# Kernel optimization log

Measured on AMD Instinct MI355X. Metric: run time of the kernel, lower is better.

## Reference

```python
import jax, jax.numpy as jnp
import numpy as np

N = 51200      # num nodes
E = 614400     # num edges
G = 256        # num graphs
T = 8          # num target capsules (GCNConv heads)
D = 128        # in_channels == out_channels
ROUTES = 3     # num_routes
BN_EPS = 1e-5


def squash(s):
    # s: (..., D). v = |s|^2/(1+|s|^2) * s/|s|
    s2 = jnp.sum(s * s, axis=-1, keepdims=True)
    return (s2 / (1.0 + s2)) * s * jax.lax.rsqrt(s2 + 1e-16)


def setup_inputs() -> dict:
    key = jax.random.key(0)
    k0, k1, k2, k3 = jax.random.split(key, 4)
    x = jax.random.normal(k0, (N, D), dtype=jnp.float32)
    edge_index = jax.random.randint(k1, (2, E), 0, N, dtype=jnp.int32)
    batch = jnp.sort(jax.random.randint(k2, (N,), 0, G, dtype=jnp.int32))
    edge_weight = jnp.ones((E,), dtype=jnp.float32)
    gamma = jnp.ones((D,), dtype=jnp.float32)
    beta = jnp.zeros((D,), dtype=jnp.float32)
    W = jax.random.normal(k3, (T, D, D), dtype=jnp.float32) * (1.0 / np.sqrt(D))
    bias = jnp.zeros((T, D), dtype=jnp.float32)
    return {"x": x, "edge_weight": edge_weight, "gamma": gamma, "beta": beta,
            "W": W, "bias": bias, "edge_index": edge_index, "batch": batch}


def reference(x, edge_weight, gamma, beta, W, bias, edge_index, batch):
    n = x.shape[0]
    row, col = edge_index[0], edge_index[1]

    # BatchNorm1d (training-mode batch stats)
    mu = jnp.mean(x, axis=0)
    var = jnp.var(x, axis=0)
    x = (x - mu) * jax.lax.rsqrt(var + BN_EPS) * gamma + beta

    # --- GCNConv per target capsule (PyG gcn_norm with self-loops) ---
    sl = jnp.arange(n, dtype=row.dtype)
    row_sl = jnp.concatenate([row, sl])
    col_sl = jnp.concatenate([col, sl])
    w_sl = jnp.concatenate([edge_weight, jnp.ones((n,), x.dtype)])
    deg = jax.ops.segment_sum(w_sl, col_sl, num_segments=n)
    dis = jnp.where(deg > 0, jax.lax.rsqrt(jnp.maximum(deg, 1e-12)), 0.0)
    norm = dis[row_sl] * w_sl * dis[col_sl]          # (E+N,)

    xW = jnp.einsum('nd,tdo->nto', x, W)             # (N, T, D)
    caps = []
    for t in range(T):  # small fixed loop over capsule heads keeps edge msgs at (E+N, D)
        msg = norm[:, None] * xW[row_sl, t]          # (E+N, D)
        caps.append(jax.ops.segment_sum(msg, col_sl, num_segments=n) + bias[t])
    u_hat = jnp.stack(caps, axis=1)                  # (N, T, D)

    # --- dynamic routing ---
    node_deg = jax.ops.segment_sum(edge_weight, row, num_segments=n)  # original edges, no self loops
    b = jnp.broadcast_to(node_deg[:, None, None], (n, T, 1))
    u_det = jax.lax.stop_gradient(u_hat)
    for _ in range(ROUTES - 1):
        c = jax.nn.softmax(b, axis=1)                               # (N, T, 1)
        s = jax.ops.segment_sum(c * u_det, batch, num_segments=G)   # (G, T, D)
        v = squash(s)[batch]                                        # (N, T, D)
        b = b + jnp.sum(u_det * v, axis=-1, keepdims=True)

    c = jax.nn.softmax(b, axis=1)
    s = jax.ops.segment_sum(c * u_hat, batch, num_segments=G)        # (G, T, D)
    cnt = jax.ops.segment_sum(jnp.ones((n,), x.dtype), batch, num_segments=G)
    x_mean = jax.ops.segment_sum(x, batch, num_segments=G) / jnp.maximum(cnt, 1.0)[:, None]
    s = s + x_mean[:, None, :]
    v = squash(s)
    # final_layer=True: per-capsule L2 norm -> (G, T)
    return jnp.sqrt(jnp.sum(v * v, axis=-1) + 1e-16)
```

## Files before the change

### kernel.cpp

```cpp
#include <hip/hip_runtime.h>
#include <hip/hip_bf16.h>
#include <math.h>

#define N_NODES 51200
#define N_EDGES 614400
#define N_GRAPHS 256
#define T_CAPS 8
#define D_DIM 128
#define BN_EPS 1e-5f
#define RCAP 352
#define NBUCK 200
#define BCAP 4096
#define EPB 1024
#define SBLK 600

__device__ inline float waveReduceSum(float v) {
#pragma unroll
  for (int off = 1; off < 64; off <<= 1) v += __shfl_xor(v, off, 64);
  return v;
}
__device__ inline float bf_lo(unsigned u) { return __uint_as_float(u << 16); }
__device__ inline float bf_hi(unsigned u) { return __uint_as_float(u & 0xffff0000u); }
__device__ inline unsigned bfbits(float f) {
  unsigned u = __float_as_uint(f);
  return (u + 0x7FFFu + ((u >> 16) & 1u)) >> 16;
}

__global__ void __launch_bounds__(256) prep(const int* __restrict__ batch,
                                            const float* __restrict__ W,
                                            int* __restrict__ start, int* __restrict__ bcur,
                                            unsigned* __restrict__ Wp,
                                            unsigned* __restrict__ WTp,
                                            float* __restrict__ rawzero) {
  int i = blockIdx.x * 256 + threadIdx.x;
  if (i < NBUCK) bcur[i] = 0;
  for (int j = i; j < 2 * N_GRAPHS * D_DIM; j += N_NODES) rawzero[j] = 0.f;
  int bn = batch[i];
  if (i == 0) {
    for (int g = 0; g <= bn; g++) start[g] = 0;
  } else {
    int bp = batch[i - 1];
    for (int g = bp + 1; g <= bn; g++) start[g] = i;
  }
  if (i == N_NODES - 1)
    for (int g = bn + 1; g <= N_GRAPHS; g++) start[g] = N_NODES;
  for (int j = i; j < 65536; j += N_NODES) {
    int t = j >> 13, r = j & 8191;
    int k = r >> 7, o = r & 127;
    float a = W[(t << 14) + (k << 8) + o];
    float b = W[(t << 14) + (k << 8) + 128 + o];
    Wp[j] = bfbits(a) | (bfbits(b) << 16);
    float2 w2 = ((const float2*)W)[(t << 13) + (o << 6) + k];
    WTp[j] = bfbits(w2.x) | (bfbits(w2.y) << 16);
  }
}

__global__ void __launch_bounds__(256) scatter_x(
    const int* __restrict__ row, const int* __restrict__ col, const float* __restrict__ ew,
    int* __restrict__ bcur, uint2* __restrict__ ebuck, const float* __restrict__ x,
    const int* __restrict__ start, float* __restrict__ rawxsum, float* __restrict__ rawxsq) {
  int bid = blockIdx.x, tid = threadIdx.x;
  if (bid < SBLK) {
    __shared__ uint2 staged[EPB];
    __shared__ int hcnt[256], lbase[256], gbase[256], wpart[4];
    unsigned rx[4], ry[4];
    int bk[4], idx[4];
    int base4 = bid * 256 + tid;
    int4 c4 = ((const int4*)col)[base4];
    int4 r4 = ((const int4*)row)[base4];
    float4 w4 = ((const float4*)ew)[base4];
    rx[0] = ((unsigned)c4.x << 16) | (unsigned)r4.x; ry[0] = bfbits(w4.x); bk[0] = c4.x >> 8;
    rx[1] = ((unsigned)c4.y << 16) | (unsigned)r4.y; ry[1] = bfbits(w4.y); bk[1] = c4.y >> 8;
    rx[2] = ((unsigned)c4.z << 16) | (unsigned)r4.z; ry[2] = bfbits(w4.z); bk[2] = c4.z >> 8;
    rx[3] = ((unsigned)c4.w << 16) | (unsigned)r4.w; ry[3] = bfbits(w4.w); bk[3] = c4.w >> 8;
    hcnt[tid] = 0;
    __syncthreads();
#pragma unroll
    for (int k = 0; k < 4; k++) idx[k] = atomicAdd(&hcnt[bk[k]], 1);
    __syncthreads();
    int v = hcnt[tid];
    int lane = tid & 63, wid = tid >> 6;
    int s = v;
#pragma unroll
    for (int off = 1; off < 64; off <<= 1) {
      int t = __shfl_up(s, off, 64);
      if (lane >= off) s += t;
    }
    if (lane == 63) wpart[wid] = s;
    if (tid < NBUCK) gbase[tid] = atomicAdd(&bcur[tid], v);
    __syncthreads();
    int add = 0;
    for (int w2 = 0; w2 < wid; w2++) add += wpart[w2];
    lbase[tid] = s + add - v;
    __syncthreads();
#pragma unroll
    for (int k = 0; k < 4; k++) staged[lbase[bk[k]] + idx[k]] = make_uint2(rx[k], ry[k]);
    __syncthreads();
    for (int i = tid; i < EPB; i += 256) {
      uint2 r = staged[i];
      int b = r.x >> 24;
      int pos = gbase[b] + (i - lbase[b]);
      if (pos < BCAP) ebuck[b * BCAP + pos] = r;
    }
    return;
  }
  int b2 = bid - SBLK;
  int g = b2 >> 2, sub = b2 & 3;
  __shared__ float ls[8][128], ls2[8][128];
  int q = tid & 31, h = tid >> 5;
  int st = start[g], en = start[g + 1];
  const float4* x4 = (const float4*)x;
  float4 s = make_float4(0.f, 0.f, 0.f, 0.f), s2 = make_float4(0.f, 0.f, 0.f, 0.f);
  for (int n = st + sub * 8 + h; n < en; n += 32) {
    float4 v = x4[n * 32 + q];
    s.x += v.x; s.y += v.y; s.z += v.z; s.w += v.w;
    s2.x += v.x * v.x; s2.y += v.y * v.y; s2.z += v.z * v.z; s2.w += v.w * v.w;
  }
  *(float4*)&ls[h][4 * q] = s;
  *(float4*)&ls2[h][4 * q] = s2;
  __syncthreads();
  if (tid < 128) {
    float a = 0.f;
#pragma unroll
    for (int hh = 0; hh < 8; hh++) a += ls[hh][tid];
    atomicAdd(&rawxsum[g * D_DIM + tid], a);
  } else {
    int d = tid - 128;
    float a = 0.f;
#pragma unroll
    for (int hh = 0; hh < 8; hh++) a += ls2[hh][d];
    atomicAdd(&rawxsq[g * D_DIM + d], a);
  }
}

__global__ void __launch_bounds__(256) bn_fin(const float* __restrict__ rawxsum,
                                              const float* __restrict__ rawxsq,
                                              const float* __restrict__ gamma,
                                              const float* __restrict__ beta,
                                              float* __restrict__ scale,
                                              float* __restrict__ shift) {
  int d = blockIdx.x;
  int tid = threadIdx.x;
  __shared__ float ls[256], ls2[256];
  ls[tid] = rawxsum[tid * D_DIM + d];
  ls2[tid] = rawxsq[tid * D_DIM + d];
  __syncthreads();
  for (int off = 128; off; off >>= 1) {
    if (tid < off) {
      ls[tid] += ls[tid + off];
      ls2[tid] += ls2[tid + off];
    }
    __syncthreads();
  }
  if (tid == 0) {
    float mu = ls[0] * (1.0f / N_NODES);
    float var = ls2[0] * (1.0f / N_NODES) - mu * mu;
    float rstd = rsqrtf(var + BN_EPS);
    float sc = gamma[d] * rstd;
    scale[d] = sc;
    shift[d] = beta[d] - mu * sc;
  }
}

__global__ void __launch_bounds__(256) build(const uint2* __restrict__ ebuck,
                                             const int* __restrict__ bcur,
                                             unsigned* __restrict__ csr,
                                             int* __restrict__ nstart, int* __restrict__ ncnt,
                                             const float* __restrict__ x,
                                             const float* __restrict__ scale,
                                             const float* __restrict__ shift,
                                             float* __restrict__ dis,
                                             __hip_bfloat162* __restrict__ y) {
  int b = blockIdx.x, tid = threadIdx.x;
  __shared__ uint2 staged[BCAP];
  __shared__ unsigned outr[BCAP];
  __shared__ int hist[256], pref[256], cur[256], wpart[4];
  __shared__ float dis_l[256];
  int cnt = min(bcur[b], BCAP);
  for (int i = tid; i < cnt; i += 256) staged[i] = ebuck[b * BCAP + i];
  hist[tid] = 0;
  __syncthreads();
  for (int i = tid; i < cnt; i += 256) {
    int dl = (staged[i].x >> 16) & 255;
    atomicAdd(&hist[dl], 1);
  }
  __syncthreads();
  int v = hist[tid];
  int lane = tid & 63, wid = tid >> 6;
  int s = v;
#pragma unroll
  for (int off = 1; off < 64; off <<= 1) {
    int t = __shfl_up(s, off, 64);
    if (lane >= off) s += t;
  }
  if (lane == 63) wpart[wid] = s;
  __syncthreads();
  int add = 0;
  for (int w2 = 0; w2 < wid; w2++) add += wpart[w2];
  int p0 = s + add - v;
  pref[tid] = p0;
  cur[tid] = p0;
  __syncthreads();
  for (int i = tid; i < cnt; i += 256) {
    uint2 r = staged[i];
    int dl = (r.x >> 16) & 255;
    int p = atomicAdd(&cur[dl], 1);
    outr[p] = ((r.x & 0xFFFFu) << 16) | r.y;
  }
  __syncthreads();
  for (int i = tid; i < cnt; i += 256) csr[b * BCAP + i] = outr[i];
  int n = b * 256 + tid;
  int hc = hist[tid];
  nstart[n] = b * BCAP + p0;
  ncnt[n] = hc;
  float sw = 0.f;
  for (int j = p0; j < p0 + hc; j++) sw += bf_lo(outr[j]);
  float dv = sw + 1.0f;
  float dn = dv > 0.f ? rsqrtf(fmaxf(dv, 1e-12f)) : 0.f;
  dis[n] = dn;
  dis_l[tid] = dn;
  __syncthreads();
  const float4* x4 = (const float4*)x;
  const float4* sc4 = (const float4*)scale;
  const float4* sh4 = (const float4*)shift;
  uint2* y2 = (uint2*)y;
  for (int i = tid; i < 256 * 32; i += 256) {
    int nl = i >> 5, l = i & 31;
    float dnl = dis_l[nl];
    float4 scv = sc4[l], shv = sh4[l];
    float4 xv = x4[(b * 256 + nl) * 32 + l];
    unsigned u0 = bfbits(dnl * (xv.x * scv.x + shv.x)) |
                  (bfbits(dnl * (xv.y * scv.y + shv.y)) << 16);
    unsigned u1 = bfbits(dnl * (xv.z * scv.z + shv.z)) |
                  (bfbits(dnl * (xv.w * scv.w + shv.w)) << 16);
    y2[(b * 256 + nl) * 32 + l] = make_uint2(u0, u1);
  }
}

__global__ void __launch_bounds__(256) node_gather(const __hip_bfloat162* __restrict__ y,
                                                   const float* __restrict__ dis,
                                                   const int* __restrict__ nstart,
                                                   const int* __restrict__ ncnt,
                                                   const unsigned* __restrict__ csr,
                                                   __hip_bfloat162* __restrict__ agg) {
  int n = blockIdx.x * 4 + (threadIdx.x >> 6);
  int lane = threadIdx.x & 63;
  int st = nstart[n], c = ncnt[n];
  float2 a = __bfloat1622float2(y[n * 64 + lane]);
  int j = 0;
  for (; j + 4 <= c; j += 4) {
    unsigned r0 = csr[st + j], r1 = csr[st + j + 1], r2 = csr[st + j + 2],
             r3 = csr[st + j + 3];
    float2 v0 = __bfloat1622float2(y[(r0 >> 16) * 64 + lane]);
    float2 v1 = __bfloat1622float2(y[(r1 >> 16) * 64 + lane]);
    float2 v2 = __bfloat1622float2(y[(r2 >> 16) * 64 + lane]);
    float2 v3 = __bfloat1622float2(y[(r3 >> 16) * 64 + lane]);
    float w0 = bf_lo(r0), w1 = bf_lo(r1), w2 = bf_lo(r2), w3 = bf_lo(r3);
    a.x += w0 * v0.x + w1 * v1.x + w2 * v2.x + w3 * v3.x;
    a.y += w0 * v0.y + w1 * v1.y + w2 * v2.y + w3 * v3.y;
  }
  for (; j < c; j++) {
    unsigned r = csr[st + j];
    float2 v = __bfloat1622float2(y[(r >> 16) * 64 + lane]);
    float w = bf_lo(r);
    a.x += w * v.x;
    a.y += w * v.y;
  }
  float dn = dis[n];
  a.x *= dn;
  a.y *= dn;
  agg[n * 64 + lane] = __float22bfloat162_rn(a);
}

__global__ void __launch_bounds__(1024) routing_fused(
    const unsigned* __restrict__ agg_bf, const int* __restrict__ start,
    const unsigned* __restrict__ Wp, const unsigned* __restrict__ WTp,
    const float* __restrict__ bias, const float* __restrict__ rawxsum,
    const float* __restrict__ scale, const float* __restrict__ shift,
    float* __restrict__ out) {
  int g = blockIdx.x;
  int tid = threadIdx.x;
  int st = start[g], c = start[g + 1] - st;

  __shared__ unsigned ag_sh[RCAP * 68];
  __shared__ float dt_sh[384][T_CAPS];
  __shared__ float ac_sh[T_CAPS][D_DIM];
  __shared__ float s_sh[T_CAPS][D_DIM];
  __shared__ float wv_sh[T_CAPS][132];
  __shared__ float csum_sh[T_CAPS], bv_sh[T_CAPS], f_sh[T_CAPS], s2p[T_CAPS][2];
  __shared__ float csp_sh[32];

  float* scratch = &dt_sh[0][0];
  const uint4* aggb4 = (const uint4*)agg_bf;
  uint4* ag4 = (uint4*)ag_sh;
  const uint2* ag2 = (const uint2*)ag_sh;

  for (int i = tid; i < T_CAPS * 132; i += 1024) (&wv_sh[0][0])[i] = 0.f;
  if (tid < T_CAPS) {
    bv_sh[tid] = 0.f;
    csum_sh[tid] = 0.125f * (float)c;
  }
  {
    int d2 = tid & 63, h = tid >> 6;
    float sx = 0.f, sy = 0.f;
    for (int n = st + h; n < st + c; n += 16) {
      unsigned u = agg_bf[n * 64 + d2];
      sx += bf_lo(u);
      sy += bf_hi(u);
    }
    scratch[h * 128 + d2 * 2] = sx;
    scratch[h * 128 + d2 * 2 + 1] = sy;
  }
  __syncthreads();
  if (tid < 128) {
    float s = 0.f;
#pragma unroll
    for (int h = 0; h < 16; h++) s += scratch[h * 128 + tid];
    s *= 0.125f;
#pragma unroll
    for (int t = 0; t < T_CAPS; t++) ac_sh[t][tid] = s;
  }
  __syncthreads();

  int tG = tid >> 7, oG = tid & 127;
  int nL = tid >> 3, tL = tid & 7;
  int tA = tid >> 7, rep = (tid >> 5) & 3, l32 = tid & 31;

  for (int iter = 0; iter < 3; iter++) {
    {
      const unsigned* Wpt = Wp + (tG << 13);
      float s = 0.f;
#pragma unroll 8
      for (int k = 0; k < 64; k++) {
        unsigned u = Wpt[(k << 7) + oG];
        s += ac_sh[tG][2 * k] * bf_lo(u) + ac_sh[tG][2 * k + 1] * bf_hi(u);
      }
      s += csum_sh[tG] * bias[(tG << 7) + oG];
      if (iter == 2) {
        float cf = (float)c;
        float ic = 1.0f / fmaxf(cf, 1.0f);
        s += (scale[oG] * rawxsum[g * D_DIM + oG] + cf * shift[oG]) * ic;
      }
      s_sh[tG][oG] = s;
      float p = waveReduceSum(s * s);
      if ((tid & 63) == 0) s2p[tG][(tid >> 6) & 1] = p;
    }
    __syncthreads();
    if (tid < T_CAPS) {
      float s2 = s2p[tid][0] + s2p[tid][1];
      float f = (s2 / (1.0f + s2)) * rsqrtf(s2 + 1e-16f);
      f_sh[tid] = f;
      if (iter == 2) out[g * T_CAPS + tid] = sqrtf(f * f * s2 + 1e-16f);
    }
    __syncthreads();
    if (iter == 2) return;
    {
      const unsigned* WTpt = WTp + (tG << 13);
      float s = 0.f;
#pragma unroll 8
      for (int k = 0; k < 64; k++) {
        unsigned u = WTpt[(k << 7) + oG];
        s += s_sh[tG][2 * k] * bf_lo(u) + s_sh[tG][2 * k + 1] * bf_hi(u);
      }
      wv_sh[tG][oG] += f_sh[tG] * s;
      float bp = bias[(tG << 7) + oG] * s_sh[tG][oG];
      bp = waveReduceSum(bp);
      if ((tid & 63) == 0) s2p[tG][(tid >> 6) & 1] = bp;
    }
    __syncthreads();
    if (tid < T_CAPS) bv_sh[tid] += f_sh[tid] * (s2p[tid][0] + s2p[tid][1]);
    __syncthreads();

    float4 acc = make_float4(0.f, 0.f, 0.f, 0.f);
    float cslr = 0.f;
    for (int cb = 0; cb < c; cb += RCAP) {
      int nv = min(RCAP, c - cb);
      for (int i = tid; i < nv * 16; i += 1024) {
        int r = i >> 4, k = i & 15;
        ag4[r * 17 + k] = aggb4[(size_t)(st + cb + r) * 16 + k];
      }
      __syncthreads();
      for (int n = nL; n < nv; n += 128) {
        float pr = 0.f;
#pragma unroll 4
        for (int k = 0; k < 16; k++) {
          uint4 u = ag4[n * 17 + k];
          float4 wa = *(const float4*)&wv_sh[tL][k * 8];
          float4 wb = *(const float4*)&wv_sh[tL][k * 8 + 4];
          pr += bf_lo(u.x) * wa.x + bf_hi(u.x) * wa.y + bf_lo(u.y) * wa.z + bf_hi(u.y) * wa.w;
          pr += bf_lo(u.z) * wb.x + bf_hi(u.z) * wb.y + bf_lo(u.w) * wb.z + bf_hi(u.w) * wb.w;
        }
        dt_sh[n][tL] = pr + bv_sh[tL];
      }
      __syncthreads();
      if (tid < nv) {
        float l0 = dt_sh[tid][0], l1 = dt_sh[tid][1], l2 = dt_sh[tid][2], l3 = dt_sh[tid][3];
        float l4 = dt_sh[tid][4], l5 = dt_sh[tid][5], l6 = dt_sh[tid][6], l7 = dt_sh[tid][7];
        float m = fmaxf(fmaxf(fmaxf(l0, l1), fmaxf(l2, l3)),
                        fmaxf(fmaxf(l4, l5), fmaxf(l6, l7)));
        float e0 = __expf(l0 - m), e1 = __expf(l1 - m), e2 = __expf(l2 - m),
              e3 = __expf(l3 - m), e4 = __expf(l4 - m), e5 = __expf(l5 - m),
              e6 = __expf(l6 - m), e7 = __expf(l7 - m);
        float iz = 1.0f / (e0 + e1 + e2 + e3 + e4 + e5 + e6 + e7);
        dt_sh[tid][0] = e0 * iz;
        dt_sh[tid][1] = e1 * iz;
        dt_sh[tid][2] = e2 * iz;
        dt_sh[tid][3] = e3 * iz;
        dt_sh[tid][4] = e4 * iz;
        dt_sh[tid][5] = e5 * iz;
        dt_sh[tid][6] = e6 * iz;
        dt_sh[tid][7] = e7 * iz;
      }
      __syncthreads();
      for (int nj = rep; nj < nv; nj += 4) {
        float cj = dt_sh[nj][tA];
        uint2 u = ag2[nj * 34 + l32];
        acc.x += cj * bf_lo(u.x);
        acc.y += cj * bf_hi(u.x);
        acc.z += cj * bf_lo(u.y);
        acc.w += cj * bf_hi(u.y);
        if (l32 == 0) cslr += cj;
      }
      __syncthreads();
    }
    int d4 = l32 << 2;
    if (rep > 0) *(float4*)&scratch[(((rep - 1) << 3) + tA) * 128 + d4] = acc;
    if (l32 == 0) csp_sh[tid >> 5] = cslr;
    __syncthreads();
    if (rep == 0) {
#pragma unroll
      for (int m = 0; m < 3; m++) {
        float4 o4 = *(const float4*)&scratch[((m << 3) + tA) * 128 + d4];
        acc.x += o4.x;
        acc.y += o4.y;
        acc.z += o4.z;
        acc.w += o4.w;
      }
      *(float4*)&ac_sh[tA][d4] = acc;
    }
    if (tid < T_CAPS)
      csum_sh[tid] = csp_sh[tid * 4] + csp_sh[tid * 4 + 1] + csp_sh[tid * 4 + 2] +
                     csp_sh[tid * 4 + 3];
    __syncthreads();
  }
}

extern "C" void kernel_launch(void* const* d_in, const int* in_sizes, int n_in, void* d_out,
                              int out_size, void* d_ws, size_t ws_size, hipStream_t stream) {
  const float* x = (const float*)d_in[0];
  const float* ew = (const float*)d_in[1];
  const float* gamma = (const float*)d_in[2];
  const float* beta = (const float*)d_in[3];
  const float* W = (const float*)d_in[4];
  const float* bias = (const float*)d_in[5];
  const int* eidx = (const int*)d_in[6];
  const int* batch = (const int*)d_in[7];
  float* out = (float*)d_out;
  float* w = (float*)d_ws;

  const int* row = eidx;
  const int* col = eidx + N_EDGES;

  int* bcur = (int*)w;
  int* start = bcur + 256;
  float* scale = (float*)(start + 260);
  float* shift = scale + 128;
  float* dis = shift + 128;
  float* rawxsum = dis + N_NODES;
  float* rawxsq = rawxsum + N_GRAPHS * D_DIM;
  unsigned* Wp = (unsigned*)(rawxsq + N_GRAPHS * D_DIM);
  unsigned* WTp = Wp + 65536;
  int* nstart = (int*)(WTp + 65536);
  int* ncnt = nstart + N_NODES;
  uint2* ebuck = (uint2*)(ncnt + N_NODES);
  unsigned* csr = (unsigned*)(ebuck + (size_t)NBUCK * BCAP);
  __hip_bfloat162* y = (__hip_bfloat162*)(csr + (size_t)NBUCK * BCAP);
  unsigned* agg_bf = (unsigned*)(y + (size_t)N_NODES * 64);

  prep<<<N_NODES / 256, 256, 0, stream>>>(batch, W, start, bcur, Wp, WTp, rawxsum);
  scatter_x<<<SBLK + 4 * N_GRAPHS, 256, 0, stream>>>(row, col, ew, bcur, ebuck, x, start,
                                                     rawxsum, rawxsq);
  bn_fin<<<D_DIM, 256, 0, stream>>>(rawxsum, rawxsq, gamma, beta, scale, shift);
  build<<<NBUCK, 256, 0, stream>>>(ebuck, bcur, csr, nstart, ncnt, x, scale, shift, dis, y);
  node_gather<<<N_NODES / 4, 256, 0, stream>>>(y, dis, nstart, ncnt, csr,
                                               (__hip_bfloat162*)agg_bf);
  routing_fused<<<N_GRAPHS, 1024, 0, stream>>>(agg_bf, start, Wp, WTp, bias, rawxsum, scale,
                                               shift, out);
}
```

Before: 202.2 us.

## Use bf16 MFMA with hi/lo split for routing logits and weighted sums

Replaces the scalar FMA loops in the routing kernel with MFMA 16x16x32 bf16 instructions, both for the node-by-capsule logit product and for the softmax-weighted aggregation. To keep accuracy, the fp32 operands (routing vector, coefficients) are split into hi and lo bf16 parts and two MFMAs are issued. It also shrinks the staging tile to 256 rows and skips reloading node features when a graph fits in one tile. This adds padding and zeroing logic and extra shared memory, and the result may differ slightly numerically.

```diff
diff --git a/kernel.cpp b/kernel.cpp
--- a/kernel.cpp
+++ b/kernel.cpp
@@ -8,11 +8,24 @@
 #define T_CAPS 8
 #define D_DIM 128
 #define BN_EPS 1e-5f
-#define RCAP 352
+#define RCAP 256
 #define NBUCK 200
 #define BCAP 4096
 #define EPB 1024
 #define SBLK 600
+
+typedef __attribute__((ext_vector_type(8))) __bf16 bf16x8;
+typedef __attribute__((ext_vector_type(8))) unsigned short ushort8;
+typedef __attribute__((ext_vector_type(4))) float f32x4;
+
+__device__ inline f32x4 mfma16(uint4 a, uint4 b, f32x4 c) {
+  return __builtin_amdgcn_mfma_f32_16x16x32_bf16(
+      __builtin_bit_cast(bf16x8, a), __builtin_bit_cast(bf16x8, b), c, 0, 0, 0);
+}
+__device__ inline f32x4 mfma16v(uint4 a, ushort8 b, f32x4 c) {
+  return __builtin_amdgcn_mfma_f32_16x16x32_bf16(
+      __builtin_bit_cast(bf16x8, a), __builtin_bit_cast(bf16x8, b), c, 0, 0, 0);
+}
 
 __device__ inline float waveReduceSum(float v) {
 #pragma unroll
@@ -287,15 +300,18 @@
   __shared__ float ac_sh[T_CAPS][D_DIM];
   __shared__ float s_sh[T_CAPS][D_DIM];
   __shared__ float wv_sh[T_CAPS][132];
+  __shared__ unsigned wvpk[2][16][68];
+  __shared__ unsigned short ctb[2][16][264];
   __shared__ float csum_sh[T_CAPS], bv_sh[T_CAPS], f_sh[T_CAPS], s2p[T_CAPS][2];
   __shared__ float csp_sh[32];
 
   float* scratch = &dt_sh[0][0];
   const uint4* aggb4 = (const uint4*)agg_bf;
   uint4* ag4 = (uint4*)ag_sh;
-  const uint2* ag2 = (const uint2*)ag_sh;
 
   for (int i = tid; i < T_CAPS * 132; i += 1024) (&wv_sh[0][0])[i] = 0.f;
+  for (int i = tid; i < 2 * 16 * 68; i += 1024) (&wvpk[0][0][0])[i] = 0u;
+  for (int i = tid; i < 2 * 16 * 264; i += 1024) (&ctb[0][0][0])[i] = 0;
   if (tid < T_CAPS) {
     bv_sh[tid] = 0.f;
     csum_sh[tid] = 0.125f * (float)c;
@@ -323,8 +339,7 @@
   __syncthreads();
 
   int tG = tid >> 7, oG = tid & 127;
-  int nL = tid >> 3, tL = tid & 7;
-  int tA = tid >> 7, rep = (tid >> 5) & 3, l32 = tid & 31;
+  int lane = tid & 63, wv_ = tid >> 6;
 
   for (int iter = 0; iter < 3; iter++) {
     {
@@ -370,78 +385,128 @@
     __syncthreads();
     if (tid < T_CAPS) bv_sh[tid] += f_sh[tid] * (s2p[tid][0] + s2p[tid][1]);
     __syncthreads();
-
-    float4 acc = make_float4(0.f, 0.f, 0.f, 0.f);
-    float cslr = 0.f;
+    for (int i = tid; i < 512; i += 1024) {
+      int t = i >> 6, kp = i & 63;
+      float a = wv_sh[t][2 * kp], b = wv_sh[t][2 * kp + 1];
+      unsigned ha = bfbits(a), hb = bfbits(b);
+      wvpk[0][t][kp] = ha | (hb << 16);
+      float ra = a - __uint_as_float(ha << 16), rb = b - __uint_as_float(hb << 16);
+      wvpk[1][t][kp] = bfbits(ra) | (bfbits(rb) << 16);
+    }
+    if (tid < 1024) {
+      (&ac_sh[0][0])[tid] = 0.f;
+    }
+    if (tid < T_CAPS) csum_sh[tid] = 0.f;
+    __syncthreads();
+
     for (int cb = 0; cb < c; cb += RCAP) {
       int nv = min(RCAP, c - cb);
-      for (int i = tid; i < nv * 16; i += 1024) {
-        int r = i >> 4, k = i & 15;
-        ag4[r * 17 + k] = aggb4[(size_t)(st + cb + r) * 16 + k];
-      }
-      __syncthreads();
-      for (int n = nL; n < nv; n += 128) {
-        float pr = 0.f;
-#pragma unroll 4
-        for (int k = 0; k < 16; k++) {
-          uint4 u = ag4[n * 17 + k];
-          float4 wa = *(const float4*)&wv_sh[tL][k * 8];
-          float4 wb = *(const float4*)&wv_sh[tL][k * 8 + 4];
-          pr += bf_lo(u.x) * wa.x + bf_hi(u.x) * wa.y + bf_lo(u.y) * wa.z + bf_hi(u.y) * wa.w;
-          pr += bf_lo(u.z) * wb.x + bf_hi(u.z) * wb.y + bf_lo(u.w) * wb.z + bf_hi(u.w) * wb.w;
-        }
-        dt_sh[n][tL] = pr + bv_sh[tL];
+      int KR32 = (nv + 31) & ~31;
+      int Mt = (nv + 15) >> 4;
+      if (iter == 0 || c > RCAP) {
+        for (int i = tid; i < nv * 16; i += 1024) {
+          int r = i >> 4, k = i & 15;
+          ag4[r * 17 + k] = aggb4[(size_t)(st + cb + r) * 16 + k];
+        }
+        for (int i = tid; i < (KR32 - nv) * 16; i += 1024) {
+          int r = nv + (i >> 4), k = i & 15;
+          ag4[r * 17 + k] = make_uint4(0, 0, 0, 0);
+        }
+        __syncthreads();
+      }
+      if (wv_ < Mt) {
+        int q = lane >> 4, tc = lane & 15;
+        int r = wv_ * 16 + tc;
+        const uint4* arow = ag4 + r * 17;
+        f32x4 C = {0.f, 0.f, 0.f, 0.f};
+#pragma unroll
+        for (int ks = 0; ks < 4; ks++) {
+          uint4 A = arow[ks * 4 + q];
+          uint4 Bh = *(const uint4*)&wvpk[0][tc][ks * 16 + 4 * q];
+          uint4 Bl = *(const uint4*)&wvpk[1][tc][ks * 16 + 4 * q];
+          C = mfma16(A, Bh, C);
+          C = mfma16(A, Bl, C);
+        }
+        if (tc < T_CAPS) {
+          float bvv = bv_sh[tc];
+#pragma unroll
+          for (int i2 = 0; i2 < 4; i2++) dt_sh[wv_ * 16 + 4 * q + i2][tc] = C[i2] + bvv;
+        }
       }
       __syncthreads();
       if (tid < nv) {
-        float l0 = dt_sh[tid][0], l1 = dt_sh[tid][1], l2 = dt_sh[tid][2], l3 = dt_sh[tid][3];
-        float l4 = dt_sh[tid][4], l5 = dt_sh[tid][5], l6 = dt_sh[tid][6], l7 = dt_sh[tid][7];
-        float m = fmaxf(fmaxf(fmaxf(l0, l1), fmaxf(l2, l3)),
-                        fmaxf(fmaxf(l4, l5), fmaxf(l6, l7)));
-        float e0 = __expf(l0 - m), e1 = __expf(l1 - m), e2 = __expf(l2 - m),
-              e3 = __expf(l3 - m), e4 = __expf(l4 - m), e5 = __expf(l5 - m),
-              e6 = __expf(l6 - m), e7 = __expf(l7 - m);
-        float iz = 1.0f / (e0 + e1 + e2 + e3 + e4 + e5 + e6 + e7);
-        dt_sh[tid][0] = e0 * iz;
-        dt_sh[tid][1] = e1 * iz;
-        dt_sh[tid][2] = e2 * iz;
-        dt_sh[tid][3] = e3 * iz;
-        dt_sh[tid][4] = e4 * iz;
-        dt_sh[tid][5] = e5 * iz;
-        dt_sh[tid][6] = e6 * iz;
-        dt_sh[tid][7] = e7 * iz;
+        float l[8];
+#pragma unroll
+        for (int t = 0; t < 8; t++) l[t] = dt_sh[tid][t];
+        float m = l[0];
+#pragma unroll
+        for (int t = 1; t < 8; t++) m = fmaxf(m, l[t]);
+        float z = 0.f;
+#pragma unroll
+        for (int t = 0; t < 8; t++) {
+          l[t] = __expf(l[t] - m);
+          z += l[t];
+        }
+        float iz = 1.0f / z;
+#pragma unroll
+        for (int t = 0; t < 8; t++) {
+          float cv = l[t] * iz;
+          dt_sh[tid][t] = cv;
+          unsigned hb = bfbits(cv);
+          ctb[0][t][tid] = (unsigned short)hb;
+          ctb[1][t][tid] = (unsigned short)bfbits(cv - __uint_as_float(hb << 16));
+        }
+      }
+      if (c > RCAP) {
+        int tail = KR32 - nv;
+        for (int i = tid; i < 16 * tail; i += 1024) {
+          int hh = i & 1, t = (i >> 1) & 7, n2 = nv + (i >> 4);
+          ctb[hh][t][n2] = 0;
+        }
       }
       __syncthreads();
-      for (int nj = rep; nj < nv; nj += 4) {
-        float cj = dt_sh[nj][tA];
-        uint2 u = ag2[nj * 34 + l32];
-        acc.x += cj * bf_lo(u.x);
-        acc.y += cj * bf_hi(u.x);
-        acc.z += cj * bf_lo(u.y);
-        acc.w += cj * bf_hi(u.y);
-        if (l32 == 0) cslr += cj;
+      {
+        int tA = tid >> 7, idx = tid & 127;
+        float p = 0.f;
+        for (int n = idx; n < nv; n += 128) p += dt_sh[n][tA];
+        p = waveReduceSum(p);
+        if (lane == 0) csp_sh[wv_] = p;
       }
       __syncthreads();
-    }
-    int d4 = l32 << 2;
-    if (rep > 0) *(float4*)&scratch[(((rep - 1) << 3) + tA) * 128 + d4] = acc;
-    if (l32 == 0) csp_sh[tid >> 5] = cslr;
-    __syncthreads();
-    if (rep == 0) {
-#pragma unroll
-      for (int m = 0; m < 3; m++) {
-        float4 o4 = *(const float4*)&scratch[((m << 3) + tA) * 128 + d4];
-        acc.x += o4.x;
-        acc.y += o4.y;
-        acc.z += o4.z;
-        acc.w += o4.w;
-      }
-      *(float4*)&ac_sh[tA][d4] = acc;
-    }
-    if (tid < T_CAPS)
-      csum_sh[tid] = csp_sh[tid * 4] + csp_sh[tid * 4 + 1] + csp_sh[tid * 4 + 2] +
-                     csp_sh[tid * 4 + 3];
-    __syncthreads();
+      if (tid < T_CAPS) csum_sh[tid] += csp_sh[2 * tid] + csp_sh[2 * tid + 1];
+      {
+        int nt = wv_ & 7, kh = wv_ >> 3;
+        int tc = lane & 15, q = lane >> 4;
+        f32x4 C = {0.f, 0.f, 0.f, 0.f};
+        const unsigned short* agh = (const unsigned short*)ag_sh;
+        int KS = KR32 >> 5;
+        for (int ks = kh; ks < KS; ks += 2) {
+          uint4 Ah = *(const uint4*)&ctb[0][tc][ks * 32 + 8 * q];
+          uint4 Al = *(const uint4*)&ctb[1][tc][ks * 32 + 8 * q];
+          int nb = ks * 32 + 8 * q, dcol = nt * 16 + tc;
+          ushort8 B;
+#pragma unroll
+          for (int j = 0; j < 8; j++) B[j] = agh[(nb + j) * 136 + dcol];
+          C = mfma16v(Ah, B, C);
+          C = mfma16v(Al, B, C);
+        }
+        if (kh == 1) *(f32x4*)&scratch[(nt * 64 + lane) * 4] = C;
+        __syncthreads();
+        if (kh == 0) {
+          f32x4 o4 = *(const f32x4*)&scratch[(nt * 64 + lane) * 4];
+          C.x += o4.x;
+          C.y += o4.y;
+          C.z += o4.z;
+          C.w += o4.w;
+#pragma unroll
+          for (int i2 = 0; i2 < 4; i2++) {
+            int tt = 4 * q + i2;
+            if (tt < T_CAPS) ac_sh[tt][nt * 16 + tc] += C[i2];
+          }
+        }
+      }
+      __syncthreads();
+    }
   }
 }
 
```

Measured after the change: 187.3 us. 7.4% less time.
